# Optimization experiments

Measured on AMD Instinct MI355X. Metric: run time of the kernel, lower is better.

The kernel has to match this reference:

```python
import jax, jax.numpy as jnp
import numpy as np

N_BLOCKS = 500000
BLOCK_DIM = 64


def setup_inputs() -> dict:
    key = jax.random.key(0)
    ks = jax.random.split(key, 7)
    d = BLOCK_DIM
    s = jax.random.normal(ks[0], (d,), dtype=jnp.float32)
    h = jax.random.normal(ks[1], (N_BLOCKS * d,), dtype=jnp.float32)
    keys = jax.random.normal(ks[2], (N_BLOCKS, d), dtype=jnp.float32)
    # xavier-uniform style scale for d x d matrices
    lim = np.sqrt(6.0 / (d + d)).astype(np.float32)
    U = jax.random.uniform(ks[3], (d, d), dtype=jnp.float32, minval=-lim, maxval=lim)
    V = jax.random.uniform(ks[4], (d, d), dtype=jnp.float32, minval=-lim, maxval=lim)
    W = jax.random.uniform(ks[5], (d, d), dtype=jnp.float32, minval=-lim, maxval=lim)
    bias = jnp.full((d,), 0.001, dtype=jnp.float32)
    prelu_a = jnp.array([0.25], dtype=jnp.float32)  # nn.PReLU() default
    return {"s": s, "h": h, "keys": keys, "U": U, "V": V, "W": W,
            "bias": bias, "prelu_a": prelu_a}


def reference(s, h, keys, U, V, W, bias, prelu_a):
    d = s.shape[0]
    hb = h.reshape(-1, d)                      # [N, d] blocks of h
    # gate: sigmoid(<s,hj> + <s,wj>) per block
    g = jax.nn.sigmoid(hb @ s + keys @ s)      # [N]
    # candidate: PReLU(U hj + V wj + W s + b), batched over blocks
    pre = hb @ U.T + keys @ V.T + (W @ s) + bias  # [N, d]
    act = jnp.where(pre >= 0, pre, prelu_a[0] * pre)
    h_new = hb + g[:, None] * act              # gated residual update
    h_new = h_new / jnp.linalg.norm(h_new, axis=1, keepdims=True)
    return h_new.reshape(-1)
```

## Files before the change

kernel.cpp:

```cpp
#include <hip/hip_runtime.h>

#define D 64
#define ROWS 64
#define TPB 256

typedef float f4 __attribute__((ext_vector_type(4)));
typedef short s8 __attribute__((ext_vector_type(8)));

static __device__ __forceinline__ unsigned short f2bf(float x) {
  union { float f; unsigned u; } v; v.f = x;
  return (unsigned short)((v.u + 0x7FFFu + ((v.u >> 16) & 1u)) >> 16);
}

static __device__ __forceinline__ s8 pack8(f4 a, f4 b) {
  s8 r;
  r[0] = (short)f2bf(a.x); r[1] = (short)f2bf(a.y);
  r[2] = (short)f2bf(a.z); r[3] = (short)f2bf(a.w);
  r[4] = (short)f2bf(b.x); r[5] = (short)f2bf(b.y);
  r[6] = (short)f2bf(b.z); r[7] = (short)f2bf(b.w);
  return r;
}

static __device__ __forceinline__ f4 fma4s(float a, f4 b, f4 c) {
  f4 r;
  r.x = fmaf(a, b.x, c.x);
  r.y = fmaf(a, b.y, c.y);
  r.z = fmaf(a, b.z, c.z);
  r.w = fmaf(a, b.w, c.w);
  return r;
}

static __device__ __forceinline__ f4 prelu4(f4 p, float a) {
  f4 r;
  r.x = p.x >= 0.0f ? p.x : a * p.x;
  r.y = p.y >= 0.0f ? p.y : a * p.y;
  r.z = p.z >= 0.0f ? p.z : a * p.z;
  r.w = p.w >= 0.0f ? p.w : a * p.w;
  return r;
}

__global__ __launch_bounds__(TPB, 2) void dmc_fused(
    const float* __restrict__ h,
    const float* __restrict__ keys,
    const float* __restrict__ s,
    const float* __restrict__ U,
    const float* __restrict__ V,
    const float* __restrict__ W,
    const float* __restrict__ bias,
    const float* __restrict__ prelu_a,
    float* __restrict__ out,
    const int nblocks) {
  __shared__ __align__(16) float hT[ROWS * D];
  __shared__ __align__(16) float kT[ROWS * D];
  __shared__ __align__(16) unsigned short Ub[D * D];
  __shared__ __align__(16) unsigned short Vb[D * D];
  __shared__ __align__(16) float cc[D];

  const int tid  = threadIdx.x;
  const int lane = tid & 63;
  const int wv   = tid >> 6;
  const int j0   = blockIdx.x * ROWS;
  const int nrem = nblocks - j0;

  const f4* __restrict__ hg = reinterpret_cast<const f4*>(h + (size_t)j0 * D);
  const f4* __restrict__ kg = reinterpret_cast<const f4*>(keys + (size_t)j0 * D);
  f4* __restrict__ hTw = reinterpret_cast<f4*>(hT);
  f4* __restrict__ kTw = reinterpret_cast<f4*>(kT);
  #pragma unroll
  for (int t = 0; t < 4; ++t) {
    const int gi = tid + TPB * t;
    const int r  = gi >> 4;
    const int ch = gi & 15;
    f4 v = {0.f, 0.f, 0.f, 0.f};
    if (r < nrem) v = hg[gi];
    hTw[r * 16 + (ch ^ (r & 15))] = v;
  }
  #pragma unroll
  for (int t = 0; t < 4; ++t) {
    const int gi = tid + TPB * t;
    const int r  = gi >> 4;
    const int ch = gi & 15;
    f4 v = {0.f, 0.f, 0.f, 0.f};
    if (r < nrem) v = kg[gi];
    kTw[r * 16 + (ch ^ (r & 15))] = v;
  }

  const f4* __restrict__ Ug = reinterpret_cast<const f4*>(U);
  const f4* __restrict__ Vg = reinterpret_cast<const f4*>(V);
  s8* __restrict__ Ub8w = reinterpret_cast<s8*>(Ub);
  s8* __restrict__ Vb8w = reinterpret_cast<s8*>(Vb);
  #pragma unroll
  for (int t = 0; t < 2; ++t) {
    const int m  = tid + TPB * t;
    const int c  = m >> 3;
    const int sl = m & 7;
    Ub8w[c * 8 + (sl ^ (c & 7))] = pack8(Ug[c * 16 + sl * 2], Ug[c * 16 + sl * 2 + 1]);
    Vb8w[c * 8 + (sl ^ (c & 7))] = pack8(Vg[c * 16 + sl * 2], Vg[c * 16 + sl * 2 + 1]);
  }

  if (tid < D) {
    const f4* __restrict__ wr = reinterpret_cast<const f4*>(W + tid * D);
    const f4* __restrict__ sr = reinterpret_cast<const f4*>(s);
    float acc = bias[tid];
    #pragma unroll
    for (int q = 0; q < 16; ++q) {
      const f4 wq = wr[q];
      const f4 sq = sr[q];
      acc = fmaf(wq.x, sq.x, acc);
      acc = fmaf(wq.y, sq.y, acc);
      acc = fmaf(wq.z, sq.z, acc);
      acc = fmaf(wq.w, sq.w, acc);
    }
    cc[tid] = acc;
  }
  __syncthreads();

  const int g  = lane >> 4;
  const int rl = lane & 15;
  const int r  = wv * 16 + rl;
  const int rbase = r * 16;
  const int rsw   = r & 15;
  const f4* __restrict__ hT4 = reinterpret_cast<const f4*>(hT);
  const f4* __restrict__ kT4 = reinterpret_cast<const f4*>(kT);
  const s8* __restrict__ Ub8 = reinterpret_cast<const s8*>(Ub);
  const s8* __restrict__ Vb8 = reinterpret_cast<const s8*>(Vb);
  const f4* __restrict__ cc4 = reinterpret_cast<const f4*>(cc);

  f4 acc0 = cc4[0 + g];
  f4 acc1 = cc4[4 + g];
  f4 acc2 = cc4[8 + g];
  f4 acc3 = cc4[12 + g];

  #pragma unroll
  for (int ks = 0; ks < 2; ++ks) {
    const int q0 = ks * 8 + g * 2;
    const f4 h0 = hT4[rbase + (q0 ^ rsw)];
    const f4 h1 = hT4[rbase + ((q0 + 1) ^ rsw)];
    const f4 k0 = kT4[rbase + (q0 ^ rsw)];
    const f4 k1 = kT4[rbase + ((q0 + 1) ^ rsw)];
    const s8 bh = pack8(h0, h1);
    const s8 bk = pack8(k0, k1);
    const int asl = ks * 4 + g;
#define CBSTEP(cb, ACC) { \
    const int c = (cb) * 16 + rl; \
    const s8 au = Ub8[c * 8 + (asl ^ (c & 7))]; \
    const s8 av = Vb8[c * 8 + (asl ^ (c & 7))]; \
    ACC = __builtin_amdgcn_mfma_f32_16x16x32_bf16(au, bh, ACC, 0, 0, 0); \
    ACC = __builtin_amdgcn_mfma_f32_16x16x32_bf16(av, bk, ACC, 0, 0, 0); }
    CBSTEP(0, acc0)
    CBSTEP(1, acc1)
    CBSTEP(2, acc2)
    CBSTEP(3, acc3)
#undef CBSTEP
  }

  float gd = 0.0f;
  const f4* __restrict__ sg4 = reinterpret_cast<const f4*>(s);
  #pragma unroll
  for (int i = 0; i < 4; ++i) {
    const int q = g * 4 + i;
    const f4 hv = hT4[rbase + (q ^ rsw)];
    const f4 kv = kT4[rbase + (q ^ rsw)];
    const f4 sv = sg4[q];
    gd = fmaf(hv.x + kv.x, sv.x, gd);
    gd = fmaf(hv.y + kv.y, sv.y, gd);
    gd = fmaf(hv.z + kv.z, sv.z, gd);
    gd = fmaf(hv.w + kv.w, sv.w, gd);
  }
  gd += __shfl_xor(gd, 16);
  gd += __shfl_xor(gd, 32);
  const float gt = 1.0f / (1.0f + __expf(-gd));
  const float a  = prelu_a[0];

  const f4 hr0 = hT4[rbase + ((0 + g) ^ rsw)];
  const f4 hr1 = hT4[rbase + ((4 + g) ^ rsw)];
  const f4 hr2 = hT4[rbase + ((8 + g) ^ rsw)];
  const f4 hr3 = hT4[rbase + ((12 + g) ^ rsw)];
  f4 o0 = fma4s(gt, prelu4(acc0, a), hr0);
  f4 o1 = fma4s(gt, prelu4(acc1, a), hr1);
  f4 o2 = fma4s(gt, prelu4(acc2, a), hr2);
  f4 o3 = fma4s(gt, prelu4(acc3, a), hr3);

  float ss = o0.x * o0.x + o0.y * o0.y + o0.z * o0.z + o0.w * o0.w;
  ss = fmaf(o1.x, o1.x, ss); ss = fmaf(o1.y, o1.y, ss);
  ss = fmaf(o1.z, o1.z, ss); ss = fmaf(o1.w, o1.w, ss);
  ss = fmaf(o2.x, o2.x, ss); ss = fmaf(o2.y, o2.y, ss);
  ss = fmaf(o2.z, o2.z, ss); ss = fmaf(o2.w, o2.w, ss);
  ss = fmaf(o3.x, o3.x, ss); ss = fmaf(o3.y, o3.y, ss);
  ss = fmaf(o3.z, o3.z, ss); ss = fmaf(o3.w, o3.w, ss);
  ss += __shfl_xor(ss, 16);
  ss += __shfl_xor(ss, 32);
  const float rn = rsqrtf(ss);

  if (r < nrem) {
    float* __restrict__ orow = out + (size_t)(j0 + r) * D + g * 4;
    *reinterpret_cast<f4*>(orow +  0) = o0 * rn;
    *reinterpret_cast<f4*>(orow + 16) = o1 * rn;
    *reinterpret_cast<f4*>(orow + 32) = o2 * rn;
    *reinterpret_cast<f4*>(orow + 48) = o3 * rn;
  }
}

extern "C" void kernel_launch(void* const* d_in, const int* in_sizes, int n_in,
                              void* d_out, int out_size, void* d_ws, size_t ws_size,
                              hipStream_t stream) {
  const float* s       = (const float*)d_in[0];
  const float* h       = (const float*)d_in[1];
  const float* keys    = (const float*)d_in[2];
  const float* U       = (const float*)d_in[3];
  const float* V       = (const float*)d_in[4];
  const float* W       = (const float*)d_in[5];
  const float* bias    = (const float*)d_in[6];
  const float* prelu_a = (const float*)d_in[7];
  float* out = (float*)d_out;

  const int nblocks = in_sizes[1] / D;
  const int grid = (nblocks + ROWS - 1) / ROWS;
  dmc_fused<<<grid, TPB, 0, stream>>>(h, keys, s, U, V, W, bias, prelu_a, out,
                                      nblocks);
}
```

Measured before the change: 110.8 us.

## Load h and keys rows directly from global, dropping LDS staging

Removes the shared-memory staging of h and keys tiles. Each lane now reads its row fragments straight from global memory into registers and feeds them to the MFMA B operand and the gate dot product. The residual is read again from global, relying on cache hits. Cutting 32KB of LDS per block allows raising the launch-bounds occupancy hint from 2 to 4 blocks per CU, at the cost of less coalesced per-lane 16B/32B global loads and a duplicate h read.

```diff
diff --git a/kernel.cpp b/kernel.cpp
--- a/kernel.cpp
+++ b/kernel.cpp
@@ -39,7 +39,15 @@
   return r;
 }
 
-__global__ __launch_bounds__(TPB, 2) void dmc_fused(
+static __device__ __forceinline__ float dot4(f4 x, f4 y, f4 z, float acc) {
+  acc = fmaf(x.x + y.x, z.x, acc);
+  acc = fmaf(x.y + y.y, z.y, acc);
+  acc = fmaf(x.z + y.z, z.z, acc);
+  acc = fmaf(x.w + y.w, z.w, acc);
+  return acc;
+}
+
+__global__ __launch_bounds__(TPB, 4) void dmc_fused(
     const float* __restrict__ h,
     const float* __restrict__ keys,
     const float* __restrict__ s,
@@ -50,8 +58,6 @@
     const float* __restrict__ prelu_a,
     float* __restrict__ out,
     const int nblocks) {
-  __shared__ __align__(16) float hT[ROWS * D];
-  __shared__ __align__(16) float kT[ROWS * D];
   __shared__ __align__(16) unsigned short Ub[D * D];
   __shared__ __align__(16) unsigned short Vb[D * D];
   __shared__ __align__(16) float cc[D];
@@ -61,29 +67,6 @@
   const int wv   = tid >> 6;
   const int j0   = blockIdx.x * ROWS;
   const int nrem = nblocks - j0;
-
-  const f4* __restrict__ hg = reinterpret_cast<const f4*>(h + (size_t)j0 * D);
-  const f4* __restrict__ kg = reinterpret_cast<const f4*>(keys + (size_t)j0 * D);
-  f4* __restrict__ hTw = reinterpret_cast<f4*>(hT);
-  f4* __restrict__ kTw = reinterpret_cast<f4*>(kT);
-  #pragma unroll
-  for (int t = 0; t < 4; ++t) {
-    const int gi = tid + TPB * t;
-    const int r  = gi >> 4;
-    const int ch = gi & 15;
-    f4 v = {0.f, 0.f, 0.f, 0.f};
-    if (r < nrem) v = hg[gi];
-    hTw[r * 16 + (ch ^ (r & 15))] = v;
-  }
-  #pragma unroll
-  for (int t = 0; t < 4; ++t) {
-    const int gi = tid + TPB * t;
-    const int r  = gi >> 4;
-    const int ch = gi & 15;
-    f4 v = {0.f, 0.f, 0.f, 0.f};
-    if (r < nrem) v = kg[gi];
-    kTw[r * 16 + (ch ^ (r & 15))] = v;
-  }
 
   const f4* __restrict__ Ug = reinterpret_cast<const f4*>(U);
   const f4* __restrict__ Vg = reinterpret_cast<const f4*>(V);
@@ -118,64 +101,70 @@
   const int g  = lane >> 4;
   const int rl = lane & 15;
   const int r  = wv * 16 + rl;
-  const int rbase = r * 16;
-  const int rsw   = r & 15;
-  const f4* __restrict__ hT4 = reinterpret_cast<const f4*>(hT);
-  const f4* __restrict__ kT4 = reinterpret_cast<const f4*>(kT);
-  const s8* __restrict__ Ub8 = reinterpret_cast<const s8*>(Ub);
-  const s8* __restrict__ Vb8 = reinterpret_cast<const s8*>(Vb);
+  const int rc = (r < nrem) ? r : (nrem - 1);
+
+  const f4* __restrict__ hrow = reinterpret_cast<const f4*>(h + (size_t)(j0 + rc) * D);
+  const f4* __restrict__ krow = reinterpret_cast<const f4*>(keys + (size_t)(j0 + rc) * D);
+  const f4* __restrict__ sg4  = reinterpret_cast<const f4*>(s);
+
+  const f4 h0a = hrow[2 * g];      const f4 h0b = hrow[2 * g + 1];
+  const f4 h1a = hrow[8 + 2 * g];  const f4 h1b = hrow[8 + 2 * g + 1];
+  const f4 k0a = krow[2 * g];      const f4 k0b = krow[2 * g + 1];
+  const f4 k1a = krow[8 + 2 * g];  const f4 k1b = krow[8 + 2 * g + 1];
+
+  float gd = 0.0f;
+  gd = dot4(h0a, k0a, sg4[2 * g], gd);
+  gd = dot4(h0b, k0b, sg4[2 * g + 1], gd);
+  gd = dot4(h1a, k1a, sg4[8 + 2 * g], gd);
+  gd = dot4(h1b, k1b, sg4[8 + 2 * g + 1], gd);
+
+  const s8 bh0 = pack8(h0a, h0b);
+  const s8 bh1 = pack8(h1a, h1b);
+  const s8 bk0 = pack8(k0a, k0b);
+  const s8 bk1 = pack8(k1a, k1b);
+
   const f4* __restrict__ cc4 = reinterpret_cast<const f4*>(cc);
-
   f4 acc0 = cc4[0 + g];
   f4 acc1 = cc4[4 + g];
   f4 acc2 = cc4[8 + g];
   f4 acc3 = cc4[12 + g];
 
+  const s8* __restrict__ Ub8 = reinterpret_cast<const s8*>(Ub);
+  const s8* __restrict__ Vb8 = reinterpret_cast<const s8*>(Vb);
   #pragma unroll
   for (int ks = 0; ks < 2; ++ks) {
-    const int q0 = ks * 8 + g * 2;
-    const f4 h0 = hT4[rbase + (q0 ^ rsw)];
-    const f4 h1 = hT4[rbase + ((q0 + 1) ^ rsw)];
-    const f4 k0 = kT4[rbase + (q0 ^ rsw)];
-    const f4 k1 = kT4[rbase + ((q0 + 1) ^ rsw)];
-    const s8 bh = pack8(h0, h1);
-    const s8 bk = pack8(k0, k1);
     const int asl = ks * 4 + g;
-#define CBSTEP(cb, ACC) { \
-    const int c = (cb) * 16 + rl; \
-    const s8 au = Ub8[c * 8 + (asl ^ (c & 7))]; \
-    const s8 av = Vb8[c * 8 + (asl ^ (c & 7))]; \
-    ACC = __builtin_amdgcn_mfma_f32_16x16x32_bf16(au, bh, ACC, 0, 0, 0); \
-    ACC = __builtin_amdgcn_mfma_f32_16x16x32_bf16(av, bk, ACC, 0, 0, 0); }
-    CBSTEP(0, acc0)
-    CBSTEP(1, acc1)
-    CBSTEP(2, acc2)
-    CBSTEP(3, acc3)
-#undef CBSTEP
-  }
-
-  float gd = 0.0f;
-  const f4* __restrict__ sg4 = reinterpret_cast<const f4*>(s);
-  #pragma unroll
-  for (int i = 0; i < 4; ++i) {
-    const int q = g * 4 + i;
-    const f4 hv = hT4[rbase + (q ^ rsw)];
-    const f4 kv = kT4[rbase + (q ^ rsw)];
-    const f4 sv = sg4[q];
-    gd = fmaf(hv.x + kv.x, sv.x, gd);
-    gd = fmaf(hv.y + kv.y, sv.y, gd);
-    gd = fmaf(hv.z + kv.z, sv.z, gd);
-    gd = fmaf(hv.w + kv.w, sv.w, gd);
-  }
+    const s8 bh = (ks == 0) ? bh0 : bh1;
+    const s8 bk = (ks == 0) ? bk0 : bk1;
+    const int c0i = 0 * 16 + rl, c1i = 1 * 16 + rl;
+    const int c2i = 2 * 16 + rl, c3i = 3 * 16 + rl;
+    const s8 au0 = Ub8[c0i * 8 + (asl ^ (c0i & 7))];
+    const s8 au1 = Ub8[c1i * 8 + (asl ^ (c1i & 7))];
+    const s8 au2 = Ub8[c2i * 8 + (asl ^ (c2i & 7))];
+    const s8 au3 = Ub8[c3i * 8 + (asl ^ (c3i & 7))];
+    const s8 av0 = Vb8[c0i * 8 + (asl ^ (c0i & 7))];
+    const s8 av1 = Vb8[c1i * 8 + (asl ^ (c1i & 7))];
+    const s8 av2 = Vb8[c2i * 8 + (asl ^ (c2i & 7))];
+    const s8 av3 = Vb8[c3i * 8 + (asl ^ (c3i & 7))];
+    acc0 = __builtin_amdgcn_mfma_f32_16x16x32_bf16(au0, bh, acc0, 0, 0, 0);
+    acc1 = __builtin_amdgcn_mfma_f32_16x16x32_bf16(au1, bh, acc1, 0, 0, 0);
+    acc2 = __builtin_amdgcn_mfma_f32_16x16x32_bf16(au2, bh, acc2, 0, 0, 0);
+    acc3 = __builtin_amdgcn_mfma_f32_16x16x32_bf16(au3, bh, acc3, 0, 0, 0);
+    acc0 = __builtin_amdgcn_mfma_f32_16x16x32_bf16(av0, bk, acc0, 0, 0, 0);
+    acc1 = __builtin_amdgcn_mfma_f32_16x16x32_bf16(av1, bk, acc1, 0, 0, 0);
+    acc2 = __builtin_amdgcn_mfma_f32_16x16x32_bf16(av2, bk, acc2, 0, 0, 0);
+    acc3 = __builtin_amdgcn_mfma_f32_16x16x32_bf16(av3, bk, acc3, 0, 0, 0);
+  }
+
   gd += __shfl_xor(gd, 16);
   gd += __shfl_xor(gd, 32);
   const float gt = 1.0f / (1.0f + __expf(-gd));
   const float a  = prelu_a[0];
 
-  const f4 hr0 = hT4[rbase + ((0 + g) ^ rsw)];
-  const f4 hr1 = hT4[rbase + ((4 + g) ^ rsw)];
-  const f4 hr2 = hT4[rbase + ((8 + g) ^ rsw)];
-  const f4 hr3 = hT4[rbase + ((12 + g) ^ rsw)];
+  const f4 hr0 = hrow[0 + g];
+  const f4 hr1 = hrow[4 + g];
+  const f4 hr2 = hrow[8 + g];
+  const f4 hr3 = hrow[12 + g];
   f4 o0 = fma4s(gt, prelu4(acc0, a), hr0);
   f4 o1 = fma4s(gt, prelu4(acc1, a), hr1);
   f4 o2 = fma4s(gt, prelu4(acc2, a), hr2);
```

After: 112.4 us. No clear change (+1.4%).
